# Performance work log

Measured on AMD Instinct MI355X. Metric: run time of the kernel, lower is better.

## Reference

```python
import jax, jax.numpy as jnp
import numpy as np

LOG_2PI = np.float32(np.log(2.0 * np.pi))
NEG_BIG = np.float32(-9e15)


def setup_inputs() -> dict:
    key = jax.random.key(0)
    ks = jax.random.split(key, 8)
    N, F_in, F_out, H = 8192, 512, 128, 16
    x = jax.random.normal(ks[0], (N, F_in), dtype=jnp.float32)
    adj = jax.random.randint(ks[1], (N, N), 0, 2, dtype=jnp.int32)
    # xavier_uniform-ish init for W (gain 1.414)
    lim = np.float32(1.414 * np.sqrt(6.0 / (F_in + F_out)))
    W = jax.random.uniform(ks[2], (F_in, F_out), jnp.float32, -lim, lim)
    # VariationalAttentionNet params: lin1(2*F_out -> H), lin21/lin22(H -> 1)
    w1 = jax.random.normal(ks[3], (H, 2 * F_out), dtype=jnp.float32) * 0.05
    b1 = jnp.zeros((H,), jnp.float32)
    w21 = jax.random.normal(ks[4], (1, H), dtype=jnp.float32) * 0.05
    b21 = jnp.zeros((1,), jnp.float32)
    w22 = jax.random.normal(ks[5], (1, H), dtype=jnp.float32) * 0.05
    b22 = jnp.zeros((1,), jnp.float32)
    return {"x": x, "adj": adj, "W": W, "w1": w1, "b1": b1,
            "w21": w21, "b21": b21, "w22": w22, "b22": b22}


def reference(x, adj, W, w1, b1, w21, b21, w22, b22):
    # h = x @ W  [N, F_out]
    h = x @ W
    # VariationalAttentionNet(h, h), eval mode: z = mu
    u = jax.nn.relu(jnp.concatenate([h, h], axis=1) @ w1.T + b1)  # [N, H]
    mu = u @ w21.T + b21   # [N, 1]
    lv = u @ w22.T + b22   # [N, 1]
    sigma = jax.nn.softplus(lv)
    z = mu
    # qmp = -(log p(z) - log q(z)); with z = mu, log q(mu) = -log(sigma) - 0.5*log(2pi)
    log_p = jnp.sum(-0.5 * z * z - 0.5 * LOG_2PI)
    log_q = jnp.sum(-jnp.log(sigma) - 0.5 * LOG_2PI)
    qmp = log_q - log_p
    # per-node score z broadcast across row, masked by adjacency, row softmax
    scores = jnp.where(adj > 0, z, NEG_BIG)          # [N, N]
    attention = jax.nn.softmax(scores, axis=1)       # [N, N] (dropout off in eval)
    h_prime = attention @ h                          # [N, F_out]
    return jax.nn.elu(h_prime), qmp
```

## Files before the change

kernel.cpp:

```cpp
#include <hip/hip_runtime.h>

typedef unsigned int u32;
typedef unsigned short u16;

#define NN 8192
#define FIN 512
#define FOUT 128
#define NH 16
#define BK 64

typedef float f32x16 __attribute__((ext_vector_type(16)));
typedef __bf16 bf16x8 __attribute__((ext_vector_type(8)));

union PackAB { u32 u[4]; bf16x8 v; };

__device__ __forceinline__ u32 rne_hi(u32 u) {
  return u + (0x7FFFu + ((u >> 16) & 1u));
}
__device__ __forceinline__ u16 f32_to_bf16(float f) {
  return (u16)(rne_hi(__float_as_uint(f)) >> 16);
}

__global__ __launch_bounds__(256) void prep_kernel(
    const float* __restrict__ W, const float* __restrict__ w1,
    u16* __restrict__ WT, float* __restrict__ w1s) {
  int b = blockIdx.x, t = threadIdx.x;
  if (b < 256) {
    int o = b * 256 + t;
    int n = o >> 9, k = o & 511;
    WT[o] = f32_to_bf16(W[k * FOUT + n]);
  } else {
    for (int e = t; e < NH * FOUT; e += 256) {
      int k = e >> 7, f = e & 127;
      w1s[e] = w1[k * 256 + f] + w1[k * 256 + 128 + f];
    }
  }
}

__global__ __launch_bounds__(256, 6) void h_kernel(
    const float* __restrict__ x, const u16* __restrict__ WT,
    float* __restrict__ Hp, int KL) {
  __shared__ u16 aS[32 * BK];
  __shared__ u16 bS[128 * BK];
  int t = threadIdx.x;
  int w = t >> 6, l = t & 63;
  int m = l & 31, kh = l >> 5;
  int tile = blockIdx.x & 255, chunk = blockIdx.x >> 8;
  int i0 = tile * 32, k0 = chunk * KL;

  int arow = t >> 4, acol = (t & 15) * 4;
  int ac = (t & 15) >> 1, ah = t & 1;
  int aoff0 = arow * BK + ((ac ^ (arow & 7)) << 3) + ah * 4;
  int aoff1 = (arow + 16) * BK + ((ac ^ ((arow + 16) & 7)) << 3) + ah * 4;
  const float* ap0 = x + (size_t)(i0 + arow) * FIN + k0 + acol;
  const float* ap1 = ap0 + (size_t)16 * FIN;
  int hrow = t >> 3, hc = t & 7;
  const u16* bp0 = WT + (size_t)hrow * FIN + k0 + hc * 8;
  int boff[4];
#pragma unroll
  for (int p = 0; p < 4; ++p) {
    int r = hrow + 32 * p;
    boff[p] = r * BK + ((hc ^ (r & 7)) << 3);
  }
  int aro = m * BK, am7 = m & 7;
  int nB = w * 32 + m;
  int bro = nB * BK, bm7 = nB & 7;

  f32x16 acc;
#pragma unroll
  for (int r = 0; r < 16; ++r) acc[r] = 0.0f;

  for (int o = 0; o < KL; o += BK) {
    float4 a0 = *(const float4*)ap0;
    float4 a1 = *(const float4*)ap1;
    uint4 h0 = *(const uint4*)bp0;
    uint4 h1 = *(const uint4*)(bp0 + 32 * (size_t)FIN);
    uint4 h2 = *(const uint4*)(bp0 + 64 * (size_t)FIN);
    uint4 h3 = *(const uint4*)(bp0 + 96 * (size_t)FIN);
    ap0 += BK; ap1 += BK; bp0 += BK;
    uint2 w0, w1v;
    w0.x = (rne_hi(__float_as_uint(a0.y)) & 0xFFFF0000u) | (rne_hi(__float_as_uint(a0.x)) >> 16);
    w0.y = (rne_hi(__float_as_uint(a0.w)) & 0xFFFF0000u) | (rne_hi(__float_as_uint(a0.z)) >> 16);
    w1v.x = (rne_hi(__float_as_uint(a1.y)) & 0xFFFF0000u) | (rne_hi(__float_as_uint(a1.x)) >> 16);
    w1v.y = (rne_hi(__float_as_uint(a1.w)) & 0xFFFF0000u) | (rne_hi(__float_as_uint(a1.z)) >> 16);
    *(uint2*)&aS[aoff0] = w0;
    *(uint2*)&aS[aoff1] = w1v;
    *(uint4*)&bS[boff[0]] = h0;
    *(uint4*)&bS[boff[1]] = h1;
    *(uint4*)&bS[boff[2]] = h2;
    *(uint4*)&bS[boff[3]] = h3;
    __syncthreads();
#pragma unroll
    for (int s = 0; s < BK; s += 16) {
      int cA = (s >> 3) + kh;
      PackAB pa, pb;
      pa.v = *(const bf16x8*)&aS[aro + ((cA ^ am7) << 3)];
      pb.v = *(const bf16x8*)&bS[bro + ((cA ^ bm7) << 3)];
      acc = __builtin_amdgcn_mfma_f32_32x32x16_bf16(pa.v, pb.v, acc, 0, 0, 0);
    }
    __syncthreads();
  }
  float* hp = Hp + (size_t)chunk * NN * FOUT;
  int col = w * 32 + m;
#pragma unroll
  for (int r = 0; r < 16; ++r) {
    int row = (r & 3) + 8 * (r >> 2) + 4 * kh;
    hp[(size_t)(i0 + row) * FOUT + col] = acc[r];
  }
}

__global__ __launch_bounds__(256) void reduceH_kernel(
    const float* __restrict__ Hp, int KSH,
    const float* __restrict__ b1, const float* __restrict__ w21,
    const float* __restrict__ b21, const float* __restrict__ w22,
    const float* __restrict__ b22, const float* __restrict__ w1s,
    u16* __restrict__ HT, float* __restrict__ qpart) {
  __shared__ float hs[32][FOUT + 4];
  __shared__ float w1l[NH][FOUT + 4];
  __shared__ float us[32][NH + 1];
  int t = threadIdx.x;
  int i0 = blockIdx.x * 32;
  float v[16];
  const float* base = Hp + (size_t)i0 * FOUT + t * 16;
#pragma unroll
  for (int e = 0; e < 16; e += 4) {
    float4 x4 = *(const float4*)(base + e);
    v[e] = x4.x; v[e + 1] = x4.y; v[e + 2] = x4.z; v[e + 3] = x4.w;
  }
  for (int c = 1; c < KSH; ++c) {
    const float* p = base + (size_t)c * NN * FOUT;
#pragma unroll
    for (int e = 0; e < 16; e += 4) {
      float4 x4 = *(const float4*)(p + e);
      v[e] += x4.x; v[e + 1] += x4.y; v[e + 2] += x4.z; v[e + 3] += x4.w;
    }
  }
  {
    int row = t >> 3, c0 = (t & 7) * 16;
#pragma unroll
    for (int e = 0; e < 16; ++e) hs[row][c0 + e] = v[e];
  }
  for (int e = t; e < NH * FOUT; e += 256) w1l[e >> 7][e & 127] = w1s[e];
  __syncthreads();
#pragma unroll
  for (int cc = 0; cc < 2; ++cc) {
    int c = cc * 64 + (t >> 2), q = t & 3;
    u32 p[4];
#pragma unroll
    for (int j = 0; j < 4; ++j) {
      u16 lo = f32_to_bf16(hs[q * 8 + 2 * j][c]);
      u16 hi = f32_to_bf16(hs[q * 8 + 2 * j + 1][c]);
      p[j] = (u32)lo | ((u32)hi << 16);
    }
    uint4 st; st.x = p[0]; st.y = p[1]; st.z = p[2]; st.w = p[3];
    *(uint4*)(HT + (size_t)c * NN + i0 + q * 8) = st;
  }
  {
    int i = t >> 3, p = t & 7;
    float s0 = b1[p], s1 = b1[p + 8];
#pragma unroll 4
    for (int f = 0; f < FOUT; ++f) {
      float hv = hs[i][f];
      s0 = fmaf(hv, w1l[p][f], s0);
      s1 = fmaf(hv, w1l[p + 8][f], s1);
    }
    us[i][p] = fmaxf(s0, 0.0f);
    us[i][p + 8] = fmaxf(s1, 0.0f);
  }
  __syncthreads();
  if (t < 32) {
    float mu = b21[0], lv = b22[0];
#pragma unroll
    for (int k = 0; k < NH; ++k) {
      mu = fmaf(us[t][k], w21[k], mu);
      lv = fmaf(us[t][k], w22[k], lv);
    }
    float sp = fmaxf(lv, 0.0f) + log1pf(expf(-fabsf(lv)));
    float q = 0.5f * mu * mu - logf(sp);
#pragma unroll
    for (int off = 16; off; off >>= 1) q += __shfl_down(q, off);
    if (t == 0) qpart[blockIdx.x] = q;
  }
}

__global__ __launch_bounds__(256, 6) void attn_kernel(
    const int* __restrict__ adj, const u16* __restrict__ HT,
    float* __restrict__ Sp, u32* __restrict__ degw, int KL) {
  __shared__ u16 aS[32 * BK];
  __shared__ u16 bS[128 * BK];
  int t = threadIdx.x;
  int w = t >> 6, l = t & 63;
  int m = l & 31, kh = l >> 5;
  int tile = blockIdx.x & 255, chunk = blockIdx.x >> 8;
  int i0 = tile * 32, k0 = chunk * KL;

  int arow = t >> 4, acol = (t & 15) * 4;
  int ac = (t & 15) >> 1, ah = t & 1;
  int aoff0 = arow * BK + ((ac ^ (arow & 7)) << 3) + ah * 4;
  int aoff1 = (arow + 16) * BK + ((ac ^ ((arow + 16) & 7)) << 3) + ah * 4;
  const int* ap0 = adj + (size_t)(i0 + arow) * NN + k0 + acol;
  const int* ap1 = ap0 + (size_t)16 * NN;
  int hrow = t >> 3, hc = t & 7;
  const u16* bp0 = HT + (size_t)hrow * NN + k0 + hc * 8;
  int boff[4];
#pragma unroll
  for (int p = 0; p < 4; ++p) {
    int r = hrow + 32 * p;
    boff[p] = r * BK + ((hc ^ (r & 7)) << 3);
  }
  int aro = m * BK, am7 = m & 7;
  int nB = w * 32 + m;
  int bro = nB * BK, bm7 = nB & 7;

  f32x16 acc;
#pragma unroll
  for (int r = 0; r < 16; ++r) acc[r] = 0.0f;
  u32 degA = 0, degB = 0;

  for (int o = 0; o < KL; o += BK) {
    int4 a0 = *(const int4*)ap0;
    int4 a1 = *(const int4*)ap1;
    uint4 h0 = *(const uint4*)bp0;
    uint4 h1 = *(const uint4*)(bp0 + 32 * (size_t)NN);
    uint4 h2 = *(const uint4*)(bp0 + 64 * (size_t)NN);
    uint4 h3 = *(const uint4*)(bp0 + 96 * (size_t)NN);
    ap0 += BK; ap1 += BK; bp0 += BK;
    u32 p00 = ((u32)a0.y << 16) | (u32)a0.x;
    u32 p01 = ((u32)a0.w << 16) | (u32)a0.z;
    u32 p10 = ((u32)a1.y << 16) | (u32)a1.x;
    u32 p11 = ((u32)a1.w << 16) | (u32)a1.z;
    degA += p00 + p01;
    degB += p10 + p11;
    uint2 w0, w1v;
    w0.x = p00 * 0x3F80u; w0.y = p01 * 0x3F80u;
    w1v.x = p10 * 0x3F80u; w1v.y = p11 * 0x3F80u;
    *(uint2*)&aS[aoff0] = w0;
    *(uint2*)&aS[aoff1] = w1v;
    *(uint4*)&bS[boff[0]] = h0;
    *(uint4*)&bS[boff[1]] = h1;
    *(uint4*)&bS[boff[2]] = h2;
    *(uint4*)&bS[boff[3]] = h3;
    __syncthreads();
#pragma unroll
    for (int s = 0; s < BK; s += 16) {
      int cA = (s >> 3) + kh;
      PackAB pa, pb;
      pa.v = *(const bf16x8*)&aS[aro + ((cA ^ am7) << 3)];
      pb.v = *(const bf16x8*)&bS[bro + ((cA ^ bm7) << 3)];
      acc = __builtin_amdgcn_mfma_f32_32x32x16_bf16(pa.v, pb.v, acc, 0, 0, 0);
    }
    __syncthreads();
  }
  u32 dA = (degA & 0xFFFFu) + (degA >> 16);
  u32 dB = (degB & 0xFFFFu) + (degB >> 16);
#pragma unroll
  for (int off = 8; off; off >>= 1) {
    dA += __shfl_down(dA, off);
    dB += __shfl_down(dB, off);
  }
  if ((t & 15) == 0) {
    degw[chunk * NN + i0 + arow] = dA;
    degw[chunk * NN + i0 + arow + 16] = dB;
  }
  float* sp = Sp + (size_t)chunk * NN * FOUT;
  int col = w * 32 + m;
#pragma unroll
  for (int r = 0; r < 16; ++r) {
    int row = (r & 3) + 8 * (r >> 2) + 4 * kh;
    sp[(size_t)(i0 + row) * FOUT + col] = acc[r];
  }
}

__global__ __launch_bounds__(256) void reduceS_kernel(
    const float* __restrict__ Sp, const u32* __restrict__ degw,
    float* __restrict__ out, int KSA) {
  int idx = (blockIdx.x * 256 + threadIdx.x) * 4;
  int i = idx >> 7;
  u32 deg = 0;
  for (int c = 0; c < KSA; ++c) deg += degw[c * NN + i];
  float4 s = {0.0f, 0.0f, 0.0f, 0.0f};
  for (int c = 0; c < KSA; ++c) {
    float4 v4 = *(const float4*)(Sp + (size_t)c * NN * FOUT + idx);
    s.x += v4.x; s.y += v4.y; s.z += v4.z; s.w += v4.w;
  }
  float rd = deg ? 1.0f / (float)deg : 0.0f;
  float4 o;
  o.x = s.x * rd; o.y = s.y * rd; o.z = s.z * rd; o.w = s.w * rd;
  o.x = o.x > 0.0f ? o.x : expm1f(o.x);
  o.y = o.y > 0.0f ? o.y : expm1f(o.y);
  o.z = o.z > 0.0f ? o.z : expm1f(o.z);
  o.w = o.w > 0.0f ? o.w : expm1f(o.w);
  *(float4*)(out + idx) = o;
}

__global__ __launch_bounds__(256) void qred_kernel(
    const float* __restrict__ qpart, float* __restrict__ outq) {
  __shared__ float sred[4];
  int t = threadIdx.x;
  float v = qpart[t];
#pragma unroll
  for (int off = 32; off; off >>= 1) v += __shfl_down(v, off);
  if ((t & 63) == 0) sred[t >> 6] = v;
  __syncthreads();
  if (t == 0) outq[0] = sred[0] + sred[1] + sred[2] + sred[3];
}

extern "C" void kernel_launch(void* const* d_in, const int* in_sizes, int n_in,
                              void* d_out, int out_size, void* d_ws, size_t ws_size,
                              hipStream_t stream) {
  (void)in_sizes; (void)n_in; (void)out_size;
  const float* x   = (const float*)d_in[0];
  const int*   adj = (const int*)d_in[1];
  const float* W   = (const float*)d_in[2];
  const float* w1  = (const float*)d_in[3];
  const float* b1  = (const float*)d_in[4];
  const float* w21 = (const float*)d_in[5];
  const float* b21 = (const float*)d_in[6];
  const float* w22 = (const float*)d_in[7];
  const float* b22 = (const float*)d_in[8];
  float* out = (float*)d_out;

  const size_t TILE4 = (size_t)NN * FOUT * 4;
  int KSA = 8, KSH = 4;
  for (;;) {
    size_t need = (size_t)(KSA + KSH) * TILE4
                + (size_t)NN * FOUT * 2
                + (size_t)FOUT * FIN * 2
                + (size_t)KSA * NN * 4
                + NH * FOUT * 4 + 2048;
    if (need <= ws_size || (KSA == 1 && KSH == 1)) break;
    if (KSH > 1) KSH >>= 1; else KSA >>= 1;
  }

  char* ws = (char*)d_ws;
  float* Sp   = (float*)ws;                          ws += (size_t)KSA * TILE4;
  float* Hp   = (float*)ws;                          ws += (size_t)KSH * TILE4;
  u16*   HT   = (u16*)ws;                            ws += (size_t)NN * FOUT * 2;
  u16*   WT   = (u16*)ws;                            ws += (size_t)FOUT * FIN * 2;
  u32*   degw = (u32*)ws;                            ws += (size_t)KSA * NN * 4;
  float* w1s  = (float*)ws;                          ws += NH * FOUT * 4;
  float* qpart= (float*)ws;

  prep_kernel<<<257, 256, 0, stream>>>(W, w1, WT, w1s);
  h_kernel<<<256 * KSH, 256, 0, stream>>>(x, WT, Hp, FIN / KSH);
  reduceH_kernel<<<256, 256, 0, stream>>>(Hp, KSH, b1, w21, b21, w22, b22, w1s, HT, qpart);
  attn_kernel<<<256 * KSA, 256, 0, stream>>>(adj, HT, Sp, degw, NN / KSA);
  reduceS_kernel<<<1024, 256, 0, stream>>>(Sp, degw, out, KSA);
  qred_kernel<<<1, 256, 0, stream>>>(qpart, out + (size_t)NN * FOUT);
}
```

Baseline: 441.3 us.

## Prefetch next adj/H slab into registers, stagger slab order, merge q-reduction kernel

The attention GEMM loop now loads the next K-slab of adjacency and H into registers right after the barrier, so global loads overlap with the MFMA work on the current slab. Each row tile also starts at a different slab (tile mod nslab) and wraps around, spreading concurrent blocks across different columns of H. The separate single-block qmp reduction kernel is folded into the final reduce kernel as an extra block, saving one launch. In exchange there is more register pressure for the prefetch buffers.

```diff
diff --git a/kernel.cpp b/kernel.cpp
--- a/kernel.cpp
+++ b/kernel.cpp
@@ -54,12 +54,12 @@
   int aoff1 = (arow + 16) * BK + ((ac ^ ((arow + 16) & 7)) << 3) + ah * 4;
   const float* ap0 = x + (size_t)(i0 + arow) * FIN + k0 + acol;
   const float* ap1 = ap0 + (size_t)16 * FIN;
-  int hrow = t >> 3, hc = t & 7;
-  const u16* bp0 = WT + (size_t)hrow * FIN + k0 + hc * 8;
+  int hr = t >> 3, hc = t & 7;
+  const u16* bp0 = WT + (size_t)hr * FIN + k0 + hc * 8;
   int boff[4];
 #pragma unroll
   for (int p = 0; p < 4; ++p) {
-    int r = hrow + 32 * p;
+    int r = hr + 32 * p;
     boff[p] = r * BK + ((hc ^ (r & 7)) << 3);
   }
   int aro = m * BK, am7 = m & 7;
@@ -193,19 +193,19 @@
   int m = l & 31, kh = l >> 5;
   int tile = blockIdx.x & 255, chunk = blockIdx.x >> 8;
   int i0 = tile * 32, k0 = chunk * KL;
+  int nslab = KL / BK;
 
   int arow = t >> 4, acol = (t & 15) * 4;
   int ac = (t & 15) >> 1, ah = t & 1;
   int aoff0 = arow * BK + ((ac ^ (arow & 7)) << 3) + ah * 4;
   int aoff1 = (arow + 16) * BK + ((ac ^ ((arow + 16) & 7)) << 3) + ah * 4;
-  const int* ap0 = adj + (size_t)(i0 + arow) * NN + k0 + acol;
-  const int* ap1 = ap0 + (size_t)16 * NN;
-  int hrow = t >> 3, hc = t & 7;
-  const u16* bp0 = HT + (size_t)hrow * NN + k0 + hc * 8;
+  const int* apb = adj + (size_t)(i0 + arow) * NN + k0 + acol;
+  int hr = t >> 3, hc = t & 7;
+  const u16* bpb = HT + (size_t)hr * NN + k0 + hc * 8;
   int boff[4];
 #pragma unroll
   for (int p = 0; p < 4; ++p) {
-    int r = hrow + 32 * p;
+    int r = hr + 32 * p;
     boff[p] = r * BK + ((hc ^ (r & 7)) << 3);
   }
   int aro = m * BK, am7 = m & 7;
@@ -217,14 +217,15 @@
   for (int r = 0; r < 16; ++r) acc[r] = 0.0f;
   u32 degA = 0, degB = 0;
 
-  for (int o = 0; o < KL; o += BK) {
-    int4 a0 = *(const int4*)ap0;
-    int4 a1 = *(const int4*)ap1;
-    uint4 h0 = *(const uint4*)bp0;
-    uint4 h1 = *(const uint4*)(bp0 + 32 * (size_t)NN);
-    uint4 h2 = *(const uint4*)(bp0 + 64 * (size_t)NN);
-    uint4 h3 = *(const uint4*)(bp0 + 96 * (size_t)NN);
-    ap0 += BK; ap1 += BK; bp0 += BK;
+  int sl = tile % nslab;
+  int4 a0 = *(const int4*)(apb + (size_t)sl * BK);
+  int4 a1 = *(const int4*)(apb + (size_t)sl * BK + (size_t)16 * NN);
+  uint4 h0 = *(const uint4*)(bpb + (size_t)sl * BK);
+  uint4 h1 = *(const uint4*)(bpb + (size_t)sl * BK + 32 * (size_t)NN);
+  uint4 h2 = *(const uint4*)(bpb + (size_t)sl * BK + 64 * (size_t)NN);
+  uint4 h3 = *(const uint4*)(bpb + (size_t)sl * BK + 96 * (size_t)NN);
+
+  for (int oo = 0; oo < nslab; ++oo) {
     u32 p00 = ((u32)a0.y << 16) | (u32)a0.x;
     u32 p01 = ((u32)a0.w << 16) | (u32)a0.z;
     u32 p10 = ((u32)a1.y << 16) | (u32)a1.x;
@@ -241,6 +242,16 @@
     *(uint4*)&bS[boff[2]] = h2;
     *(uint4*)&bS[boff[3]] = h3;
     __syncthreads();
+    if (oo + 1 < nslab) {
+      int s2 = sl + 1 == nslab ? 0 : sl + 1;
+      sl = s2;
+      a0 = *(const int4*)(apb + (size_t)s2 * BK);
+      a1 = *(const int4*)(apb + (size_t)s2 * BK + (size_t)16 * NN);
+      h0 = *(const uint4*)(bpb + (size_t)s2 * BK);
+      h1 = *(const uint4*)(bpb + (size_t)s2 * BK + 32 * (size_t)NN);
+      h2 = *(const uint4*)(bpb + (size_t)s2 * BK + 64 * (size_t)NN);
+      h3 = *(const uint4*)(bpb + (size_t)s2 * BK + 96 * (size_t)NN);
+    }
 #pragma unroll
     for (int s = 0; s < BK; s += 16) {
       int cA = (s >> 3) + kh;
@@ -271,10 +282,21 @@
   }
 }
 
-__global__ __launch_bounds__(256) void reduceS_kernel(
+__global__ __launch_bounds__(256) void reduceSq_kernel(
     const float* __restrict__ Sp, const u32* __restrict__ degw,
-    float* __restrict__ out, int KSA) {
-  int idx = (blockIdx.x * 256 + threadIdx.x) * 4;
+    const float* __restrict__ qpart, float* __restrict__ out, int KSA) {
+  int t = threadIdx.x;
+  if (blockIdx.x == 1024) {
+    __shared__ float sred[4];
+    float v = qpart[t];
+#pragma unroll
+    for (int off = 32; off; off >>= 1) v += __shfl_down(v, off);
+    if ((t & 63) == 0) sred[t >> 6] = v;
+    __syncthreads();
+    if (t == 0) out[(size_t)NN * FOUT] = sred[0] + sred[1] + sred[2] + sred[3];
+    return;
+  }
+  int idx = (blockIdx.x * 256 + t) * 4;
   int i = idx >> 7;
   u32 deg = 0;
   for (int c = 0; c < KSA; ++c) deg += degw[c * NN + i];
@@ -291,18 +313,6 @@
   o.z = o.z > 0.0f ? o.z : expm1f(o.z);
   o.w = o.w > 0.0f ? o.w : expm1f(o.w);
   *(float4*)(out + idx) = o;
-}
-
-__global__ __launch_bounds__(256) void qred_kernel(
-    const float* __restrict__ qpart, float* __restrict__ outq) {
-  __shared__ float sred[4];
-  int t = threadIdx.x;
-  float v = qpart[t];
-#pragma unroll
-  for (int off = 32; off; off >>= 1) v += __shfl_down(v, off);
-  if ((t & 63) == 0) sred[t >> 6] = v;
-  __syncthreads();
-  if (t == 0) outq[0] = sred[0] + sred[1] + sred[2] + sred[3];
 }
 
 extern "C" void kernel_launch(void* const* d_in, const int* in_sizes, int n_in,
@@ -345,6 +355,5 @@
   h_kernel<<<256 * KSH, 256, 0, stream>>>(x, WT, Hp, FIN / KSH);
   reduceH_kernel<<<256, 256, 0, stream>>>(Hp, KSH, b1, w21, b21, w22, b22, w1s, HT, qpart);
   attn_kernel<<<256 * KSA, 256, 0, stream>>>(adj, HT, Sp, degw, NN / KSA);
-  reduceS_kernel<<<1024, 256, 0, stream>>>(Sp, degw, out, KSA);
-  qred_kernel<<<1, 256, 0, stream>>>(qpart, out + (size_t)NN * FOUT);
-}
+  reduceSq_kernel<<<1025, 256, 0, stream>>>(Sp, degw, qpart, out, KSA);
+}
```

New measurement: 437.3 us. Within noise of the previous version (-0.9%).
